# Performance work log

Measured on AMD Instinct MI355X. Metric: run time of the kernel, lower is better.

Reference implementation:

```python
import jax, jax.numpy as jnp
import numpy as np
import math

CHUNK = 32
NS_STEPS = 5
MAX_GNORM = 10.0


def _normalize(x, eps=1e-12):
    n = jnp.linalg.norm(x, axis=-1, keepdims=True)
    return x / jnp.maximum(n, eps)


def _poly(x):  # poly_degree = 2: [x, x^2] / sqrt(2)
    return jnp.concatenate([x, x * x], axis=-1) / math.sqrt(2.0)


def _ns5(G):
    # Muon-style Newton-Schulz orthogonalization (quintic, 5 steps)
    a, b, c = 3.4445, -4.7750, 2.0315
    t = G.shape[0] > G.shape[1]
    X = G.T if t else G
    X = X / (jnp.linalg.norm(X) + 1e-7)
    for _ in range(NS_STEPS):
        A = X @ X.T
        B = b * A + c * (A @ A)
        X = a * X + B @ X
    return X.T if t else X


def _clip_mean(g):
    # per-sample grad-norm clipping to MAX_GNORM, then mean over samples
    n = g.shape[0]
    norms = jnp.maximum(jnp.linalg.norm(g.reshape(n, -1), axis=1), 1e-8)
    scale = jnp.maximum(norms / MAX_GNORM, 1.0)
    return jnp.mean(g / scale.reshape((n,) + (1,) * (g.ndim - 1)), axis=0)


def _mem_fwd(W0, W1, z):  # MemoryMLP depth=2, gelu (exact) between layers
    return jax.nn.gelu(z @ W0, approximate=False) @ W1


def setup_inputs() -> dict:
    key = jax.random.key(0)
    ks = jax.random.split(key, 16)
    B, S, D, M, P, H = 2, 1024, 2048, 512, 1024, 2048
    w = lambda k, shape, fan_in: jax.random.normal(k, shape, jnp.float32) / np.float32(np.sqrt(fan_in))
    return {
        "x": jax.random.normal(ks[0], (B, S, D), jnp.float32),
        "Wk": w(ks[1], (M, D), D),
        "Wv": w(ks[2], (M, D), D),
        "Wq": w(ks[3], (M, D), D),
        "Wout": w(ks[4], (D, M), M),
        "w_lr": w(ks[5], (1, D), D), "b_lr": jnp.full((1,), -4.0, jnp.float32),
        "w_mom": w(ks[6], (1, D), D), "b_mom": jnp.full((1,), 1.0, jnp.float32),
        "w_dec": w(ks[7], (1, D), D), "b_dec": jnp.full((1,), -3.0, jnp.float32),
        "w_gate": w(ks[8], (1, D), D), "b_gate": jnp.full((1,), -1.0, jnp.float32),
        "Wmem0": w(ks[9], (P, H), P),
        "Wmem1": w(ks[10], (H, P), H),
        "Wmemout": w(ks[11], (P, M), P),
        "Wvexp": w(ks[12], (M, P), M),
    }


def reference(x, Wk, Wv, Wq, Wout, w_lr, b_lr, w_mom, b_mom, w_dec, b_dec,
              w_gate, b_gate, Wmem0, Wmem1, Wmemout, Wvexp):
    # Inference path (torch.is_grad_enabled() == False): chunked ATLAS update.
    B, S, D = x.shape
    NC = S // CHUNK

    k = _normalize(x @ Wk.T)          # (B,S,M)
    v = x @ Wv.T                       # (B,S,M)
    q = _normalize(x @ Wq.T)          # (B,S,M)
    kp = _poly(k)                      # (B,S,P)
    qp = _poly(q)                      # (B,S,P)
    vexp = v @ Wvexp                   # v_expand: (B,S,P)

    gate = lambda w, b: jax.nn.sigmoid(jnp.einsum('bsd,od->bso', x, w) + b)
    lr, mom, dec, og = gate(w_lr, b_lr), gate(w_mom, b_mom), gate(w_dec, b_dec), gate(w_gate, b_gate)

    cmean = lambda t: t[..., 0].reshape(B, NC, CHUNK).mean(axis=(0, 2))  # per-chunk scalar
    lr_c, mom_c, dec_c = cmean(lr), cmean(mom), cmean(dec)

    chunks = lambda t: t.reshape(B, NC, CHUNK, t.shape[-1]).transpose(1, 0, 2, 3)  # (NC,B,C,F)
    qc, kc, vc = chunks(qp), chunks(kp), chunks(vexp)

    def loss_fn(params, kk, vv):  # ||M(k) - v||^2 per sample
        W0_, W1_ = params
        pred = jax.nn.gelu(kk @ W0_, approximate=False) @ W1_
        return jnp.sum((pred - vv) ** 2)

    grad_fn = jax.vmap(jax.grad(loss_fn), in_axes=((None, None), 0, 0))

    def step(carry, xs):
        W0, W1, S0, S1 = carry
        qch, kch, vch, lrc, momc, decc = xs
        retr = _mem_fwd(W0, W1, qch) @ Wmemout  # retrieve with pre-update params: (B,C,M)
        kf = kch.reshape(-1, kch.shape[-1])
        vf = vch.reshape(-1, vch.shape[-1])
        g0, g1 = grad_fn((W0, W1), kf, vf)      # per-sample grads
        g0, g1 = _clip_mean(g0), _clip_mean(g1)
        s0 = momc * S0 - lrc * g0                # surprise momentum
        s1 = momc * S1 - lrc * g1
        W0n = (1.0 - decc) * W0 + _ns5(s0) * lrc # forget gate + orthogonalized step
        W1n = (1.0 - decc) * W1 + _ns5(s1) * lrc
        return (W0n, W1n, s0, s1), retr

    init = (Wmem0, Wmem1, jnp.zeros_like(Wmem0), jnp.zeros_like(Wmem1))
    _, retrs = jax.lax.scan(step, init, (qc, kc, vc, lr_c, mom_c, dec_c))
    retrieved = retrs.transpose(1, 0, 2, 3).reshape(B, S, -1)  # (B,S,M)
    delta = retrieved @ Wout.T
    return x + delta * og
```

## Files before the change

### kernel.cpp

```cpp
#include <hip/hip_runtime.h>


typedef unsigned short us;
typedef __attribute__((ext_vector_type(8))) short s16x8;
typedef __attribute__((ext_vector_type(8))) unsigned short u16x8;
typedef __attribute__((ext_vector_type(4))) float f32x4;

#define MKP 72

__device__ __forceinline__ float gelu_f(float x) {
  return 0.5f * x * (1.0f + erff(x * 0.70710678118654752f));
}
__device__ __forceinline__ float gelu_grad_f(float x) {
  float cdf = 0.5f * (1.0f + erff(x * 0.70710678118654752f));
  float pdf = 0.3989422804014327f * expf(-0.5f * x * x);
  return cdf + x * pdf;
}
__device__ __forceinline__ float sigmoid_f(float x) { return 1.0f / (1.0f + expf(-x)); }

__device__ __forceinline__ us f2bf(float f) {
  union { float f; unsigned u; } v; v.f = f;
  unsigned r = (v.u + 0x7FFFu + ((v.u >> 16) & 1u)) >> 16;
  return (us)r;
}
__device__ __forceinline__ float bf2f(us h) {
  union { unsigned u; float f; } v; v.u = ((unsigned)h) << 16;
  return v.f;
}
__device__ __forceinline__ int cm_map(int n) {
  return ((n & 1023) >> 5) * 64 + (n >> 10) * 32 + (n & 31);
}
__device__ __forceinline__ size_t pf_off(int r, int k, int KB) {
  return ((size_t)(r >> 4) * KB + (k >> 5)) * 512 + ((k >> 3) & 3) * 128 + (r & 15) * 8 + (k & 7);
}

__device__ __forceinline__ float block_reduce_sum(float v, float* red) {
  int t = threadIdx.x;
  red[t] = v; __syncthreads();
  for (int s = blockDim.x >> 1; s > 0; s >>= 1) {
    if (t < s) red[t] += red[t + s];
    __syncthreads();
  }
  float r = red[0];
  __syncthreads();
  return r;
}

__device__ __forceinline__ void gemm_pk(const us* __restrict__ A,
                                        const us* __restrict__ B, int KB,
                                        int lane, int m0, int n0,
                                        f32x4 (&acc)[4][4]) {
  const us* am[4];
  const us* bm[4];
#pragma unroll
  for (int q = 0; q < 4; ++q) {
    am[q] = A + (size_t)((m0 >> 4) + q) * KB * 512 + lane * 8;
    bm[q] = B + (size_t)((n0 >> 4) + q) * KB * 512 + lane * 8;
  }
#pragma unroll
  for (int i = 0; i < 4; ++i)
#pragma unroll
    for (int j = 0; j < 4; ++j) acc[i][j] = (f32x4){0.f, 0.f, 0.f, 0.f};
  u16x8 a0[4], b0[4], a1[4], b1[4];
#pragma unroll
  for (int q = 0; q < 4; ++q) {
    a0[q] = *(const u16x8*)(am[q]);
    b0[q] = *(const u16x8*)(bm[q]);
    a1[q] = *(const u16x8*)(am[q] + 512);
    b1[q] = *(const u16x8*)(bm[q] + 512);
  }
  for (int kb = 0; kb < KB; kb += 2) {
#pragma unroll
    for (int mi = 0; mi < 4; ++mi)
#pragma unroll
      for (int ni = 0; ni < 4; ++ni)
        acc[mi][ni] = __builtin_amdgcn_mfma_f32_16x16x32_bf16(
            (s16x8)a0[mi], (s16x8)b0[ni], acc[mi][ni], 0, 0, 0);
    if (kb + 2 < KB) {
#pragma unroll
      for (int q = 0; q < 4; ++q) {
        a0[q] = *(const u16x8*)(am[q] + (size_t)(kb + 2) * 512);
        b0[q] = *(const u16x8*)(bm[q] + (size_t)(kb + 2) * 512);
      }
    }
#pragma unroll
    for (int mi = 0; mi < 4; ++mi)
#pragma unroll
      for (int ni = 0; ni < 4; ++ni)
        acc[mi][ni] = __builtin_amdgcn_mfma_f32_16x16x32_bf16(
            (s16x8)a1[mi], (s16x8)b1[ni], acc[mi][ni], 0, 0, 0);
    if (kb + 3 < KB) {
#pragma unroll
      for (int q = 0; q < 4; ++q) {
        a1[q] = *(const u16x8*)(am[q] + (size_t)(kb + 3) * 512);
        b1[q] = *(const u16x8*)(bm[q] + (size_t)(kb + 3) * 512);
      }
    }
  }
}

template<int EPI, int TM, int TN>
__global__ __launch_bounds__(256)
void mgp_k(const us* __restrict__ Aq, const us* __restrict__ Bq,
           us* __restrict__ Cq, us* __restrict__ C2q, const us* __restrict__ Eq,
           int K, int N, float c1, float c2,
           long sA, long sB, long sC, long sE) {
  __shared__ __align__(16) us ct[4 * 64 * 72];
  const int tid = threadIdx.x;
  const int wave = tid >> 6, lane = tid & 63;
  const int l15 = lane & 15, l4 = lane >> 4;
  const int wm = (wave >> 1) * 64, wn = (wave & 1) * 64;
  const int TPB = TM * TN;
  const int t = blockIdx.x;
  const int bz = t / TPB;
  const int ti = t - bz * TPB;
  const int m0 = (ti / TN) * 128 + wm;
  const int n0 = (ti % TN) * 128 + wn;

  const us* A = Aq + (size_t)bz * sA;
  const us* B = Bq + (size_t)bz * sB;
  us* C = Cq + (size_t)bz * sC;
  us* C2 = C2q + (size_t)bz * sC;
  const us* E = Eq + (size_t)bz * sE;
  const int KB = K >> 5;

  f32x4 acc[4][4];
  gemm_pk(A, B, KB, lane, m0, n0, acc);

  us* cw = ct + wave * 64 * 72;
#pragma unroll
  for (int mi = 0; mi < 4; ++mi)
#pragma unroll
    for (int i = 0; i < 4; ++i)
#pragma unroll
      for (int ni = 0; ni < 4; ++ni)
        cw[(mi * 16 + l4 * 4 + i) * 72 + ni * 16 + l15] = f2bf(acc[mi][ni][i]);

  if constexpr (EPI == 20 || EPI == 21) {
    const int KC = N >> 5;
#pragma unroll
    for (int q = 0; q < 8; ++q) {
      u16x8 v = *(const u16x8*)&cw[lane * 72 + q * 8];
      size_t off = pf_off(m0 + lane, n0 + q * 8, KC);
      if constexpr (EPI == 21) {
        u16x8 e = *(const u16x8*)(E + off);
        u16x8 o;
#pragma unroll
        for (int w = 0; w < 8; ++w) o[w] = f2bf(c1 * bf2f(v[w]) + c2 * bf2f(e[w]));
        *(u16x8*)(C + off) = o;
      } else {
        *(u16x8*)(C + off) = v;
      }
    }
  } else if constexpr (EPI == 23) {
#pragma unroll
    for (int q = 0; q < 8; ++q) {
      size_t off = pf_off(m0 + lane, n0 + q * 8, 64);
      u16x8 v = *(const u16x8*)&cw[lane * 72 + q * 8];
      u16x8 e = *(const u16x8*)(E + off);
      u16x8 o;
#pragma unroll
      for (int w = 0; w < 8; ++w) o[w] = f2bf(bf2f(v[w]) + c1 * bf2f(e[w]));
      *(u16x8*)&cw[lane * 72 + q * 8] = o;
      *(u16x8*)(C + off) = o;
    }
#pragma unroll
    for (int q = 0; q < 8; ++q) {
      u16x8 o;
#pragma unroll
      for (int w = 0; w < 8; ++w) o[w] = cw[(q * 8 + w) * 72 + lane];
      size_t offT = pf_off(n0 + lane, m0 + q * 8, 32);
      *(u16x8*)(C2 + offT) = o;
    }
  } else {
#pragma unroll
    for (int q = 0; q < 8; ++q) {
      size_t off = pf_off(m0 + lane, n0 + q * 8, 64);
      u16x8 v = *(const u16x8*)&cw[lane * 72 + q * 8];
      u16x8 e = *(const u16x8*)(E + off);
      u16x8 o;
#pragma unroll
      for (int w = 0; w < 8; ++w) o[w] = f2bf(bf2f(v[w]) + c1 * bf2f(e[w]));
      *(u16x8*)(C + (size_t)(m0 + lane) * 2048 + n0 + q * 8) = o;
    }
  }
}

template<int EPI, int TM, int TN>
static void mgp(hipStream_t st, const us* A, const us* B, us* C, us* C2,
                const us* E, int K, int N, float c1, float c2,
                long sA, long sB, long sC, long sE) {
  dim3 g(TM * TN * 2), b(256);
  hipLaunchKernelGGL((mgp_k<EPI, TM, TN>), g, b, 0, st, A, B, C, C2, E,
                     K, N, c1, c2, sA, sB, sC, sE);
}

template<int EPI>
__device__ __forceinline__ void epilogue(f32x4 (&acc)[4][4], int m0, int n0,
    int l15, int l4, void* Cq, void* C2, const void* Eq,
    const float* FX, const float* OG, const float* cp, int cidx,
    int ldc, int lde, float c1, float c2) {
#pragma unroll
  for (int mi = 0; mi < 4; ++mi) {
#pragma unroll
    for (int i = 0; i < 4; ++i) {
      int grow = m0 + mi * 16 + l4 * 4 + i;
#pragma unroll
      for (int ni = 0; ni < 4; ++ni) {
        int col = n0 + ni * 16 + l15;
        float v = acc[mi][ni][i];
        if constexpr (EPI == 5) {
          ((us*)Cq)[(size_t)grow * ldc + col] = f2bf(v);
        } else if constexpr (EPI == 7) {
          ((float*)Cq)[(size_t)grow * ldc + col] = v;
        } else if constexpr (EPI == 8) {
          ((us*)Cq)[(size_t)grow * ldc + col] = f2bf(gelu_f(v));
          if (m0 >= 64)
            ((float*)C2)[(size_t)(grow - 64) * ldc + col] = gelu_grad_f(v);
        } else if constexpr (EPI == 9) {
          if (m0 < 64)
            ((us*)Cq)[(size_t)grow * ldc + col] = f2bf(v);
          else
            ((us*)Cq)[(size_t)grow * ldc + col] =
                f2bf(2.0f * (v - ((const float*)Eq)[(size_t)(grow - 64) * lde + col]));
        } else if constexpr (EPI == 13) {
          ((float*)Cq)[(size_t)grow * ldc + col] =
              v * ((const float*)Eq)[(size_t)grow * lde + col];
        } else if constexpr (EPI == 14) {
          float* C = (float*)Cq;
          float old = C[(size_t)grow * ldc + col];
          C[(size_t)grow * ldc + col] = cp[cidx * 3 + 1] * old - cp[cidx * 3 + 0] * v;
        } else if constexpr (EPI == 15) {
          ((float*)Cq)[(size_t)grow * ldc + col] =
              FX[(size_t)grow * ldc + col] + v * OG[grow];
        } else if constexpr (EPI == 17) {
          int crow = cm_map(grow);
          ((float*)Cq)[(size_t)crow * ldc + col] = v;
        }
      }
    }
  }
}

template<int EPI, int TA, int DUAL, int AG>
__global__ __launch_bounds__(64)
void mg_k(const us* __restrict__ Aq, const us* __restrict__ A2,
          const us* __restrict__ Bq, void* __restrict__ Cq,
          void* __restrict__ C2, const void* __restrict__ Eq,
          const float* __restrict__ FX, const float* __restrict__ OG,
          const float* __restrict__ cp, int cidx,
          int M, int N, int K, int lda, int ldb, int ldc, int lde,
          float c1, float c2) {
  __shared__ __align__(16) us As[64 * MKP];
  __shared__ __align__(16) us Bs[64 * MKP];
  const us* A = Aq;
  const us* B = Bq;
  const int t = threadIdx.x;
  const int m0 = blockIdx.y * 64, n0 = blockIdx.x * 64;
  if constexpr (DUAL) { if (m0 >= 64) A = A2; }
  const int mA0 = DUAL ? (m0 & 63) : m0;
  const int l15 = t & 15, l4 = t >> 4;

  f32x4 acc[4][4];
#pragma unroll
  for (int i = 0; i < 4; ++i)
#pragma unroll
    for (int j = 0; j < 4; ++j) acc[i][j] = (f32x4){0.f, 0.f, 0.f, 0.f};

  const int srw = t >> 3;
  const int sck = (t & 7) * 8;

  u16x8 ra[8], rb[8];
  auto LDA = [&](int k0) {
#pragma unroll
    for (int p = 0; p < 8; ++p) {
      if constexpr (TA == 0) {
        int row = srw + p * 8;
        int srow;
        if constexpr (AG) srow = cm_map(m0 + row); else srow = mA0 + row;
        ra[p] = *(const u16x8*)(A + (size_t)srow * lda + k0 + sck);
      } else {
        ra[p] = *(const u16x8*)(A + (size_t)(k0 + srw + p * 8) * lda + mA0 + sck);
      }
    }
  };
  auto LDB = [&](int k0) {
#pragma unroll
    for (int p = 0; p < 8; ++p)
      rb[p] = *(const u16x8*)(B + (size_t)(n0 + srw + p * 8) * ldb + k0 + sck);
  };

  LDA(0); LDB(0);
  for (int k0 = 0; k0 < K; k0 += 64) {
    if constexpr (TA == 0) {
#pragma unroll
      for (int p = 0; p < 8; ++p)
        *(u16x8*)&As[(srw + p * 8) * MKP + sck] = ra[p];
    } else {
#pragma unroll
      for (int p = 0; p < 8; ++p) {
        int kk = srw + p * 8;
#pragma unroll
        for (int j = 0; j < 8; ++j) As[(sck + j) * MKP + kk] = ra[p][j];
      }
    }
#pragma unroll
    for (int p = 0; p < 8; ++p)
      *(u16x8*)&Bs[(srw + p * 8) * MKP + sck] = rb[p];
    if (k0 + 64 < K) { LDA(k0 + 64); LDB(k0 + 64); }
#pragma unroll
    for (int ks = 0; ks < 2; ++ks) {
      s16x8 af[4], bf[4];
#pragma unroll
      for (int mi = 0; mi < 4; ++mi)
        af[mi] = *(const s16x8*)&As[(mi * 16 + l15) * MKP + ks * 32 + l4 * 8];
#pragma unroll
      for (int ni = 0; ni < 4; ++ni)
        bf[ni] = *(const s16x8*)&Bs[(ni * 16 + l15) * MKP + ks * 32 + l4 * 8];
#pragma unroll
      for (int mi = 0; mi < 4; ++mi)
#pragma unroll
        for (int ni = 0; ni < 4; ++ni)
          acc[mi][ni] = __builtin_amdgcn_mfma_f32_16x16x32_bf16(af[mi], bf[ni], acc[mi][ni], 0, 0, 0);
    }
  }

  epilogue<EPI>(acc, m0, n0, l15, l4, Cq, C2, Eq, FX, OG, cp, cidx,
                ldc, lde, c1, c2);
}

template<int EPI, int TA = 0, int DUAL = 0, int AG = 0>
static void mg(hipStream_t st, const us* A, const us* A2, const us* B,
               void* C, void* C2, const void* E,
               const float* FX, const float* OG, const float* cp, int cidx,
               int M, int N, int K, int lda, int ldb, int ldc, int lde,
               float c1 = 0.f, float c2 = 0.f) {
  dim3 g(N / 64, M / 64, 1), b(64);
  hipLaunchKernelGGL((mg_k<EPI, TA, DUAL, AG>), g, b, 0, st, A, A2, B, C, C2, E,
                     FX, OG, cp, cidx, M, N, K, lda, ldb, ldc, lde, c1, c2);
}

__global__ void scalepk2_k(const float* __restrict__ S0, const float* __restrict__ S1,
                           const float* __restrict__ inv01,
                           us* __restrict__ XP, us* __restrict__ XTP) {
  __shared__ float tile[32][33];
  const long SB2c = 2097152;
  int z = blockIdx.z;
  float s = inv01[z];
  int tx = threadIdx.x, ty = threadIdx.y;
  int r0, c0;
  const float* S;
  if (z == 0) { S = S0; c0 = blockIdx.x * 32; r0 = blockIdx.y * 32; }
  else        { S = S1; r0 = blockIdx.x * 32; c0 = blockIdx.y * 32; }
  int C = (z == 0) ? 2048 : 1024;
#pragma unroll
  for (int j = 0; j < 4; ++j)
    tile[ty + 8 * j][tx] = S[(size_t)(r0 + ty + 8 * j) * C + c0 + tx] * s;
  __syncthreads();
  us* xp = XP + (size_t)z * SB2c;
  us* xt = XTP + (size_t)z * SB2c;
  int t = ty * 32 + tx;
  if (t < 128) {
    int rh = t >> 2, cc = t & 3;
    u16x8 v;
#pragma unroll
    for (int e = 0; e < 8; ++e) v[e] = f2bf(tile[rh][cc * 8 + e]);
    if (z == 0) {
      *(u16x8*)(xp + pf_off(r0 + rh, c0 + cc * 8, 64)) = v;
    } else {
      *(u16x8*)(xt + pf_off(r0 + rh, c0 + cc * 8, 32)) = v;
    }
  } else {
    int ch = (t - 128) >> 2, rc = (t - 128) & 3;
    u16x8 v;
#pragma unroll
    for (int e = 0; e < 8; ++e) v[e] = f2bf(tile[rc * 8 + e][ch]);
    if (z == 0) {
      *(u16x8*)(xt + pf_off(c0 + ch, r0 + rc * 8, 32)) = v;
    } else {
      *(u16x8*)(xp + pf_off(c0 + ch, r0 + rc * 8, 64)) = v;
    }
  }
}


__global__ __launch_bounds__(256) void conv_k(const float* __restrict__ in,
                                              us* __restrict__ out, int n) {
  for (int i = blockIdx.x * 256 + threadIdx.x; i < n; i += gridDim.x * 256)
    out[i] = f2bf(in[i]);
}

__global__ void tconv_k(const float* __restrict__ in, us* __restrict__ out, int R, int C) {
  __shared__ float tile[32][33];
  int c0 = blockIdx.x * 32, r0 = blockIdx.y * 32;
  int tx = threadIdx.x, ty = threadIdx.y;
#pragma unroll
  for (int j = 0; j < 4; ++j)
    tile[ty + 8 * j][tx] = in[(size_t)(r0 + ty + 8 * j) * C + c0 + tx];
  __syncthreads();
#pragma unroll
  for (int j = 0; j < 4; ++j)
    out[(size_t)(c0 + ty + 8 * j) * R + r0 + tx] = f2bf(tile[tx][ty + 8 * j]);
}


__global__ __launch_bounds__(256) void polynorm2_k(const float* __restrict__ lin,
                                                   us* __restrict__ outp) {
  __shared__ float red[256];
  int n = blockIdx.x, t = threadIdx.x;
  int rowp = cm_map(n);
  float s = 0.f;
  for (int f = t; f < 512; f += 256) { float v = lin[(size_t)n * 512 + f]; s += v * v; }
  float tot = block_reduce_sum(s, red);
  float sc = 1.0f / fmaxf(sqrtf(tot), 1e-12f);
  const float is2 = 0.70710678118654752f;
  for (int f = t; f < 512; f += 256) {
    float v = lin[(size_t)n * 512 + f] * sc;
    outp[(size_t)rowp * 1024 + f] = f2bf(v * is2);
    outp[(size_t)rowp * 1024 + 512 + f] = f2bf(v * v * is2);
  }
}

__global__ __launch_bounds__(256) void gates_k(const float* __restrict__ x,
    const float* __restrict__ wlr, const float* __restrict__ blr,
    const float* __restrict__ wmom, const float* __restrict__ bmom,
    const float* __restrict__ wdec, const float* __restrict__ bdec,
    const float* __restrict__ wgate, const float* __restrict__ bgate,
    float* __restrict__ lrv, float* __restrict__ momv,
    float* __restrict__ decv, float* __restrict__ og) {
  __shared__ float red[256];
  int n = blockIdx.x, t = threadIdx.x;
  float s0 = 0.f, s1 = 0.f, s2 = 0.f, s3 = 0.f;
  for (int d = t; d < 2048; d += 256) {
    float xv = x[(size_t)n * 2048 + d];
    s0 += xv * wlr[d]; s1 += xv * wmom[d]; s2 += xv * wdec[d]; s3 += xv * wgate[d];
  }
  float r0 = block_reduce_sum(s0, red);
  float r1 = block_reduce_sum(s1, red);
  float r2 = block_reduce_sum(s2, red);
  float r3 = block_reduce_sum(s3, red);
  if (t == 0) {
    lrv[n] = sigmoid_f(r0 + blr[0]);
    momv[n] = sigmoid_f(r1 + bmom[0]);
    decv[n] = sigmoid_f(r2 + bdec[0]);
    og[n] = sigmoid_f(r3 + bgate[0]);
  }
}

__global__ void chunk_means_k(const float* __restrict__ lrv, const float* __restrict__ momv,
                              const float* __restrict__ decv, float* __restrict__ cp) {
  int c = blockIdx.x, t = threadIdx.x;
  int n = ((t >> 5) << 10) + c * 32 + (t & 31);
  float a = lrv[n], b = momv[n], d = decv[n];
  for (int off = 32; off > 0; off >>= 1) {
    a += __shfl_down(a, off);
    b += __shfl_down(b, off);
    d += __shfl_down(d, off);
  }
  if (t == 0) {
    cp[c * 3 + 0] = a * (1.f / 64.f);
    cp[c * 3 + 1] = b * (1.f / 64.f);
    cp[c * 3 + 2] = d * (1.f / 64.f);
  }
}

__global__ __launch_bounds__(256) void sampnorm2_k(const us* __restrict__ kp_b,
                                                   const float* __restrict__ dh,
                                                   const us* __restrict__ hab,
                                                   const us* __restrict__ pr,
                                                   float* __restrict__ w0inv,
                                                   float* __restrict__ w1inv, int c) {
  __shared__ float red[256];
  int i = blockIdx.x, t = threadIdx.x;
  int row = c * 64 + i;
  float sk = 0.f, sr = 0.f, sdh = 0.f, sa = 0.f;
  for (int p = t; p < 1024; p += 256) {
    float v = bf2f(kp_b[(size_t)row * 1024 + p]); sk += v * v;
    v = bf2f(pr[(size_t)(64 + i) * 1024 + p]); sr += v * v;
  }
  for (int h = t; h < 2048; h += 256) {
    float v = dh[(size_t)i * 2048 + h]; sdh += v * v;
    v = bf2f(hab[(size_t)(64 + i) * 2048 + h]); sa += v * v;
  }
  float tk = block_reduce_sum(sk, red);
  float tdh = block_reduce_sum(sdh, red);
  float ta = block_reduce_sum(sa, red);
  float tr = block_reduce_sum(sr, red);
  if (t == 0) {
    float n0 = fmaxf(sqrtf(tk) * sqrtf(tdh), 1e-8f);
    w0inv[i] = 1.0f / (64.0f * fmaxf(n0 * 0.1f, 1.0f));
    float n1 = fmaxf(sqrtf(ta) * sqrtf(tr), 1e-8f);
    w1inv[i] = 1.0f / (64.0f * fmaxf(n1 * 0.1f, 1.0f));
  }
}

template<int INF32>
__global__ void wtrans_k(const void* __restrict__ in, const float* __restrict__ w,
                         us* __restrict__ out, int C, int ldin) {
  __shared__ float tile[32][33];
  int c0 = blockIdx.x * 32, r0 = blockIdx.y * 32;
  int tx = threadIdx.x, ty = threadIdx.y;
#pragma unroll
  for (int j = 0; j < 4; ++j) {
    int r = r0 + ty + 8 * j, cc = c0 + tx;
    float v;
    if constexpr (INF32) v = ((const float*)in)[(size_t)r * ldin + cc];
    else v = bf2f(((const us*)in)[(size_t)r * ldin + cc]);
    tile[ty + 8 * j][tx] = v * w[r];
  }
  __syncthreads();
#pragma unroll
  for (int j = 0; j < 4; ++j)
    out[(size_t)(c0 + ty + 8 * j) * 64 + r0 + tx] = f2bf(tile[tx][ty + 8 * j]);
}

__global__ __launch_bounds__(256) void frob2_k(const float* __restrict__ s0,
                                               const float* __restrict__ s1, int n,
                                               float* __restrict__ parts) {
  __shared__ float red[256];
  const float* s = blockIdx.z ? s1 : s0;
  float acc = 0.f;
  for (int i = blockIdx.x * 256 + threadIdx.x; i < n; i += gridDim.x * 256) {
    float v = s[i]; acc += v * v;
  }
  float r = block_reduce_sum(acc, red);
  if (threadIdx.x == 0) parts[blockIdx.z * 256 + blockIdx.x] = r;
}

__global__ __launch_bounds__(256) void frob_fin2_k(const float* __restrict__ parts,
                                                   float* __restrict__ inv) {
  __shared__ float red[256];
  float r = block_reduce_sum(parts[blockIdx.x * 256 + threadIdx.x], red);
  if (threadIdx.x == 0) inv[blockIdx.x] = 1.0f / (sqrtf(r) + 1e-7f);
}

__global__ void wupd0_k(float* __restrict__ W0, const us* __restrict__ X,
                        us* __restrict__ W0bT, const float* __restrict__ cp, int c) {
  __shared__ float tl[32][33];
  float lr = cp[c * 3 + 0], om = 1.0f - cp[c * 3 + 2];
  int c0 = blockIdx.x * 32, r0 = blockIdx.y * 32;
  int tx = threadIdx.x, ty = threadIdx.y;
#pragma unroll
  for (int j = 0; j < 4; ++j) {
    int r = r0 + ty + 8 * j, h = c0 + tx;
    size_t idx = (size_t)r * 2048 + h;
    float v = om * W0[idx] + lr * bf2f(X[idx]);
    W0[idx] = v;
    tl[ty + 8 * j][tx] = v;
  }
  __syncthreads();
#pragma unroll
  for (int j = 0; j < 4; ++j)
    W0bT[(size_t)(c0 + ty + 8 * j) * 1024 + r0 + tx] = f2bf(tl[tx][ty + 8 * j]);
}

__global__ void wupd1_k(float* __restrict__ W1, const us* __restrict__ X2,
                        us* __restrict__ W1b, us* __restrict__ W1bT,
                        const float* __restrict__ cp, int c) {
  __shared__ float tX[32][33];
  __shared__ float t2[32][33];
  float lr = cp[c * 3 + 0], om = 1.0f - cp[c * 3 + 2];
  int h0 = blockIdx.x * 32, p0 = blockIdx.y * 32;
  int tx = threadIdx.x, ty = threadIdx.y;
#pragma unroll
  for (int j = 0; j < 4; ++j)
    tX[ty + 8 * j][tx] = bf2f(X2[(size_t)(p0 + ty + 8 * j) * 2048 + h0 + tx]);
  __syncthreads();
#pragma unroll
  for (int j = 0; j < 4; ++j) {
    int h = h0 + ty + 8 * j, p = p0 + tx;
    size_t idx = (size_t)h * 1024 + p;
    float v = om * W1[idx] + lr * tX[tx][ty + 8 * j];
    W1[idx] = v;
    W1b[idx] = f2bf(v);
    t2[tx][ty + 8 * j] = v;
  }
  __syncthreads();
#pragma unroll
  for (int j = 0; j < 4; ++j)
    W1bT[(size_t)(p0 + ty + 8 * j) * 2048 + h0 + tx] = f2bf(t2[ty + 8 * j][tx]);
}


extern "C" void kernel_launch(void* const* d_in, const int* in_sizes, int n_in,
                              void* d_out, int out_size, void* d_ws, size_t ws_size,
                              hipStream_t stream) {
  const float* x = (const float*)d_in[0];
  const float* Wk = (const float*)d_in[1];
  const float* Wv = (const float*)d_in[2];
  const float* Wq = (const float*)d_in[3];
  const float* Wout = (const float*)d_in[4];
  const float* w_lr = (const float*)d_in[5];
  const float* b_lr = (const float*)d_in[6];
  const float* w_mom = (const float*)d_in[7];
  const float* b_mom = (const float*)d_in[8];
  const float* w_dec = (const float*)d_in[9];
  const float* b_dec = (const float*)d_in[10];
  const float* w_gate = (const float*)d_in[11];
  const float* b_gate = (const float*)d_in[12];
  const float* Wmem0 = (const float*)d_in[13];
  const float* Wmem1 = (const float*)d_in[14];
  const float* Wmemout = (const float*)d_in[15];
  const float* Wvexp = (const float*)d_in[16];
  float* out = (float*)d_out;
  (void)n_in; (void)in_sizes; (void)out_size;

  const long F = 1048576;
  const long BIG = 2097152;
  const long SB2 = 2097152, SB1 = 1048576;
  float* ws = (float*)d_ws;
  if (ws_size < (size_t)25043464 * sizeof(float)) return;

  us* kp_b   = (us*)ws;
  us* qp_b   = (us*)(ws + F);
  float* vexp = ws + 2 * F;
  float* W0  = ws + 4 * F;
  float* W1  = ws + 6 * F;
  float* S0  = ws + 8 * F;
  float* S1  = ws + 10 * F;
  us* XPong  = (us*)(ws + 12 * F);
  us* XTPong = (us*)(ws + 14 * F);
  us* XPing  = (us*)(ws + 16 * F);
  us* AP     = (us*)(ws + 18 * F);
  float* SCR = ws + 19 * F;
  us* XTPing = (us*)(ws + 20 * F);
  us* BP     = (us*)(ws + 22 * F);
  us* W0bT   = (us*)(ws + 20 * F);
  us* W1bT   = (us*)(ws + 21 * F);
  us* W1b    = (us*)(ws + 22 * F);
  us* WmoT   = (us*)(ws + 23 * F);
  us* retrv  = (us*)(ws + 23 * F + 262144);
  float* smal = ws + 23 * F + 262144 + 524288;
  float* og   = smal;
  float* lrv  = og + 2048;
  float* momv = lrv + 2048;
  float* decv = momv + 2048;
  float* cpb  = decv + 2048;
  float* w0inv = cpb + 128;
  float* w1inv = w0inv + 64;
  float* parts = w1inv + 64;
  float* inv01 = parts + 512;

  us* xb   = XPong;
  us* Wkb  = XTPong;
  us* Wqb  = XTPong + 1048576;
  us* Wvb  = XTPong + 2097152;
  us* vlin = XPing;
  us* WvexpT = XPing + 1048576;
  us* Woutb = AP;
  float* lin = SCR;
  us* hab   = (us*)SCR;
  float* gp = SCR + 131072;
  us* pr    = (us*)(SCR + 262144);
  float* dh = SCR + 327680;
  us* dhT   = (us*)(SCR + 458752);
  us* rbwT  = (us*)(SCR + 524288);
  us* Xfin  = XPong;

  const float NSa = 3.4445f, NSb = -4.7750f, NSc = 2.0315f;

  hipMemcpyAsync(W0, Wmem0, (size_t)BIG * 4, hipMemcpyDeviceToDevice, stream);
  hipMemcpyAsync(W1, Wmem1, (size_t)BIG * 4, hipMemcpyDeviceToDevice, stream);
  hipMemsetAsync(S0, 0, (size_t)BIG * 4, stream);
  hipMemsetAsync(S1, 0, (size_t)BIG * 4, stream);
  hipLaunchKernelGGL(tconv_k, dim3(64, 32), dim3(32, 8), 0, stream, Wmem0, W0bT, 1024, 2048);
  hipLaunchKernelGGL(conv_k, dim3(1024), dim3(256), 0, stream, Wmem1, W1b, (int)BIG);
  hipLaunchKernelGGL(tconv_k, dim3(32, 64), dim3(32, 8), 0, stream, Wmem1, W1bT, 2048, 1024);
  hipLaunchKernelGGL(tconv_k, dim3(16, 32), dim3(32, 8), 0, stream, Wmemout, WmoT, 1024, 512);
  hipLaunchKernelGGL(tconv_k, dim3(32, 16), dim3(32, 8), 0, stream, Wvexp, WvexpT, 512, 1024);
  hipLaunchKernelGGL(conv_k, dim3(2048), dim3(256), 0, stream, x, xb, 2048 * 2048);
  hipLaunchKernelGGL(conv_k, dim3(512), dim3(256), 0, stream, Wk, Wkb, 512 * 2048);
  hipLaunchKernelGGL(conv_k, dim3(512), dim3(256), 0, stream, Wq, Wqb, 512 * 2048);
  hipLaunchKernelGGL(conv_k, dim3(512), dim3(256), 0, stream, Wv, Wvb, 512 * 2048);

  mg<7>(stream, xb, nullptr, Wkb, lin, nullptr, nullptr, nullptr, nullptr, nullptr, 0,
        2048, 512, 2048, 2048, 2048, 512, 0);
  hipLaunchKernelGGL(polynorm2_k, dim3(2048), dim3(256), 0, stream, lin, kp_b);
  mg<7>(stream, xb, nullptr, Wqb, lin, nullptr, nullptr, nullptr, nullptr, nullptr, 0,
        2048, 512, 2048, 2048, 2048, 512, 0);
  hipLaunchKernelGGL(polynorm2_k, dim3(2048), dim3(256), 0, stream, lin, qp_b);
  mg<5>(stream, xb, nullptr, Wvb, vlin, nullptr, nullptr, nullptr, nullptr, nullptr, 0,
        2048, 512, 2048, 2048, 2048, 512, 0);
  mg<17>(stream, vlin, nullptr, WvexpT, vexp, nullptr, nullptr, nullptr, nullptr, nullptr, 0,
         2048, 1024, 512, 512, 512, 1024, 0);

  hipLaunchKernelGGL(gates_k, dim3(2048), dim3(256), 0, stream, x,
                     w_lr, b_lr, w_mom, b_mom, w_dec, b_dec, w_gate, b_gate,
                     lrv, momv, decv, og);
  hipLaunchKernelGGL(chunk_means_k, dim3(32), dim3(64), 0, stream, lrv, momv, decv, cpb);

  for (int c = 0; c < 32; ++c) {
    const us* kp_c = kp_b + (size_t)c * 64 * 1024;
    const us* qp_c = qp_b + (size_t)c * 64 * 1024;
    const float* vexp_c = vexp + (size_t)c * 64 * 1024;
    mg<8, 0, 1>(stream, qp_c, kp_c, W0bT, hab, gp, nullptr, nullptr, nullptr, nullptr, 0,
                128, 2048, 1024, 1024, 1024, 2048, 0);
    mg<9>(stream, hab, nullptr, W1bT, pr, nullptr, vexp_c, nullptr, nullptr, nullptr, 0,
          128, 1024, 2048, 2048, 2048, 1024, 1024);
    mg<5>(stream, pr, nullptr, WmoT, retrv + (size_t)c * 64 * 512, nullptr, nullptr,
          nullptr, nullptr, nullptr, 0, 64, 512, 1024, 1024, 1024, 512, 0);
    mg<13>(stream, pr + 64 * 1024, nullptr, W1b, dh, nullptr, gp, nullptr, nullptr, nullptr, 0,
           64, 2048, 1024, 1024, 1024, 2048, 2048);
    hipLaunchKernelGGL(sampnorm2_k, dim3(64), dim3(256), 0, stream,
                       kp_b, dh, hab, pr, w0inv, w1inv, c);
    hipLaunchKernelGGL((wtrans_k<1>), dim3(64, 2), dim3(32, 8), 0, stream, dh, w0inv, dhT, 2048, 2048);
    hipLaunchKernelGGL((wtrans_k<0>), dim3(32, 2), dim3(32, 8), 0, stream, pr + 64 * 1024, w1inv,
                       rbwT, 1024, 1024);
    mg<14, 1>(stream, kp_c, nullptr, dhT, S0, nullptr, nullptr, nullptr, nullptr, cpb, c,
              1024, 2048, 64, 1024, 64, 2048, 0);
    mg<14, 1>(stream, hab + 64 * 2048, nullptr, rbwT, S1, nullptr, nullptr, nullptr, nullptr, cpb, c,
              2048, 1024, 64, 2048, 64, 1024, 0);

    hipLaunchKernelGGL(frob2_k, dim3(256, 1, 2), dim3(256), 0, stream, S0, S1, (int)BIG, parts);
    hipLaunchKernelGGL(frob_fin2_k, dim3(2), dim3(256), 0, stream, parts, inv01);
    hipLaunchKernelGGL(scalepk2_k, dim3(64, 32, 2), dim3(32, 8), 0, stream,
                       S0, S1, inv01, XPing, XTPing);

    us* xpA[2] = {XPing, XPong};
    us* xtA[2] = {XTPing, XTPong};
    int cur = 0;
    for (int it = 0; it < 5; ++it) {
      const us* XPc = xpA[cur];
      const us* XTPc = xtA[cur];
      int nxt = cur ^ 1;
      mgp<20, 8, 8>(stream, XPc, XPc, AP, nullptr, nullptr, 2048, 1024,
                    0.f, 0.f, SB2, SB2, SB1, 0);
      mgp<21, 8, 8>(stream, AP, AP, BP, nullptr, AP, 1024, 1024,
                    NSc, NSb, SB1, SB1, SB1, SB1);
      if (it < 4) {
        mgp<23, 8, 16>(stream, BP, XTPc, xpA[nxt], xtA[nxt], XPc, 1024, 2048,
                       NSa, 0.f, SB1, SB2, SB2, SB2);
        cur = nxt;
      } else {
        mgp<24, 8, 16>(stream, BP, XTPc, Xfin, nullptr, XPc, 1024, 2048,
                       NSa, 0.f, SB1, SB2, SB2, SB2);
      }
    }
    hipLaunchKernelGGL(wupd0_k, dim3(64, 32), dim3(32, 8), 0, stream, W0, Xfin, W0bT, cpb, c);
    hipLaunchKernelGGL(wupd1_k, dim3(64, 32), dim3(32, 8), 0, stream, W1, Xfin + SB2, W1b, W1bT, cpb, c);
  }

  hipLaunchKernelGGL(conv_k, dim3(1024), dim3(256), 0, stream, Wout, Woutb, 2048 * 512);
  mg<15, 0, 0, 1>(stream, retrv, nullptr, Woutb, out, nullptr, nullptr, x, og, nullptr, 0,
                  2048, 2048, 512, 512, 512, 2048, 0);
}
```

Before: 15.80 ms.

## Exploit symmetry in Newton-Schulz Gram products and merge per-chunk kernel launches

The X·Xᵀ and A·A products in the Newton-Schulz loop are symmetric, so only upper-triangular 128x128 tiles are computed and off-diagonal tiles are mirrored into the transposed position. This roughly halves the MFMA work for two of the three GEMMs per iteration. The two transpose kernels and the two momentum-update GEMMs are each merged into a single launch to cut launch overhead. The triangular tile index is decoded with a small loop per block, and mirrored writes add some uncoalesced-style transposed stores.

```diff
diff --git a/kernel.cpp b/kernel.cpp
--- a/kernel.cpp
+++ b/kernel.cpp
@@ -99,7 +99,7 @@
   }
 }
 
-template<int EPI, int TM, int TN>
+template<int EPI, int TRI, int TM, int TN>
 __global__ __launch_bounds__(256)
 void mgp_k(const us* __restrict__ Aq, const us* __restrict__ Bq,
            us* __restrict__ Cq, us* __restrict__ C2q, const us* __restrict__ Eq,
@@ -110,12 +110,29 @@
   const int wave = tid >> 6, lane = tid & 63;
   const int l15 = lane & 15, l4 = lane >> 4;
   const int wm = (wave >> 1) * 64, wn = (wave & 1) * 64;
-  const int TPB = TM * TN;
-  const int t = blockIdx.x;
-  const int bz = t / TPB;
-  const int ti = t - bz * TPB;
-  const int m0 = (ti / TN) * 128 + wm;
-  const int n0 = (ti % TN) * 128 + wn;
+  int bz, m0, n0;
+  bool mir = false;
+  if constexpr (TRI) {
+    const int per = TM * (TM + 1) / 2;
+    int t = blockIdx.x;
+    bz = t / per;
+    int ti = t - bz * per;
+    int m0t, n0t;
+    if (ti < TM) { m0t = n0t = ti * 128; }
+    else {
+      int p = ti - TM, i = 0;
+      while (p >= TM - 1 - i) { p -= TM - 1 - i; ++i; }
+      m0t = i * 128; n0t = (i + 1 + p) * 128; mir = true;
+    }
+    m0 = m0t + wm; n0 = n0t + wn;
+  } else {
+    const int TPB = TM * TN;
+    int t = blockIdx.x;
+    bz = t / TPB;
+    int ti = t - bz * TPB;
+    m0 = (ti / TN) * 128 + wm;
+    n0 = (ti % TN) * 128 + wn;
+  }
 
   const us* A = Aq + (size_t)bz * sA;
   const us* B = Bq + (size_t)bz * sB;
@@ -152,6 +169,24 @@
         *(u16x8*)(C + off) = v;
       }
     }
+    if (TRI && mir) {
+#pragma unroll
+      for (int q = 0; q < 8; ++q) {
+        u16x8 vT;
+#pragma unroll
+        for (int w = 0; w < 8; ++w) vT[w] = cw[(q * 8 + w) * 72 + lane];
+        size_t offM = pf_off(n0 + lane, m0 + q * 8, KC);
+        if constexpr (EPI == 21) {
+          u16x8 e = *(const u16x8*)(E + offM);
+          u16x8 o;
+#pragma unroll
+          for (int w = 0; w < 8; ++w) o[w] = f2bf(c1 * bf2f(vT[w]) + c2 * bf2f(e[w]));
+          *(u16x8*)(C + offM) = o;
+        } else {
+          *(u16x8*)(C + offM) = vT;
+        }
+      }
+    }
   } else if constexpr (EPI == 23) {
 #pragma unroll
     for (int q = 0; q < 8; ++q) {
@@ -186,12 +221,12 @@
   }
 }
 
-template<int EPI, int TM, int TN>
+template<int EPI, int TRI, int TM, int TN>
 static void mgp(hipStream_t st, const us* A, const us* B, us* C, us* C2,
                 const us* E, int K, int N, float c1, float c2,
                 long sA, long sB, long sC, long sE) {
-  dim3 g(TM * TN * 2), b(256);
-  hipLaunchKernelGGL((mgp_k<EPI, TM, TN>), g, b, 0, st, A, B, C, C2, E,
+  dim3 g(TRI ? TM * (TM + 1) : TM * TN * 2), b(256);
+  hipLaunchKernelGGL((mgp_k<EPI, TRI, TM, TN>), g, b, 0, st, A, B, C, C2, E,
                      K, N, c1, c2, sA, sB, sC, sE);
 }
 
@@ -243,6 +278,87 @@
 }
 
 template<int EPI, int TA, int DUAL, int AG>
+__device__ __forceinline__ void mg_body(const us* __restrict__ A0,
+    const us* __restrict__ A2, const us* __restrict__ B,
+    void* __restrict__ Cq, void* __restrict__ C2, const void* __restrict__ Eq,
+    const float* __restrict__ FX, const float* __restrict__ OG,
+    const float* __restrict__ cp, int cidx, int m0, int n0,
+    int K, int lda, int ldb, int ldc, int lde, float c1, float c2,
+    us* As, us* Bs, int t) {
+  const us* A = A0;
+  if constexpr (DUAL) { if (m0 >= 64) A = A2; }
+  const int mA0 = DUAL ? (m0 & 63) : m0;
+  const int l15 = t & 15, l4 = t >> 4;
+
+  f32x4 acc[4][4];
+#pragma unroll
+  for (int i = 0; i < 4; ++i)
+#pragma unroll
+    for (int j = 0; j < 4; ++j) acc[i][j] = (f32x4){0.f, 0.f, 0.f, 0.f};
+
+  const int srw = t >> 3;
+  const int sck = (t & 7) * 8;
+
+  u16x8 ra[8], rb[8];
+  auto LDA = [&](int k0) {
+#pragma unroll
+    for (int p = 0; p < 8; ++p) {
+      if constexpr (TA == 0) {
+        int row = srw + p * 8;
+        int srow;
+        if constexpr (AG) srow = cm_map(m0 + row); else srow = mA0 + row;
+        ra[p] = *(const u16x8*)(A + (size_t)srow * lda + k0 + sck);
+      } else {
+        ra[p] = *(const u16x8*)(A + (size_t)(k0 + srw + p * 8) * lda + mA0 + sck);
+      }
+    }
+  };
+  auto LDB = [&](int k0) {
+#pragma unroll
+    for (int p = 0; p < 8; ++p)
+      rb[p] = *(const u16x8*)(B + (size_t)(n0 + srw + p * 8) * ldb + k0 + sck);
+  };
+
+  LDA(0); LDB(0);
+  for (int k0 = 0; k0 < K; k0 += 64) {
+    if constexpr (TA == 0) {
+#pragma unroll
+      for (int p = 0; p < 8; ++p)
+        *(u16x8*)&As[(srw + p * 8) * MKP + sck] = ra[p];
+    } else {
+#pragma unroll
+      for (int p = 0; p < 8; ++p) {
+        int kk = srw + p * 8;
+#pragma unroll
+        for (int j = 0; j < 8; ++j) As[(sck + j) * MKP + kk] = ra[p][j];
+      }
+    }
+#pragma unroll
+    for (int p = 0; p < 8; ++p)
+      *(u16x8*)&Bs[(srw + p * 8) * MKP + sck] = rb[p];
+    if (k0 + 64 < K) { LDA(k0 + 64); LDB(k0 + 64); }
+#pragma unroll
+    for (int ks = 0; ks < 2; ++ks) {
+      s16x8 af[4], bf[4];
+#pragma unroll
+      for (int mi = 0; mi < 4; ++mi)
+        af[mi] = *(const s16x8*)&As[(mi * 16 + l15) * MKP + ks * 32 + l4 * 8];
+#pragma unroll
+      for (int ni = 0; ni < 4; ++ni)
+        bf[ni] = *(const s16x8*)&Bs[(ni * 16 + l15) * MKP + ks * 32 + l4 * 8];
+#pragma unroll
+      for (int mi = 0; mi < 4; ++mi)
+#pragma unroll
+        for (int ni = 0; ni < 4; ++ni)
+          acc[mi][ni] = __builtin_amdgcn_mfma_f32_16x16x32_bf16(af[mi], bf[ni], acc[mi][ni], 0, 0, 0);
+    }
+  }
+
+  epilogue<EPI>(acc, m0, n0, l15, l4, Cq, C2, Eq, FX, OG, cp, cidx,
+                ldc, lde, c1, c2);
+}
+
+template<int EPI, int TA, int DUAL, int AG>
 __global__ __launch_bounds__(64)
 void mg_k(const us* __restrict__ Aq, const us* __restrict__ A2,
           const us* __restrict__ Bq, void* __restrict__ Cq,
@@ -253,80 +369,9 @@
           float c1, float c2) {
   __shared__ __align__(16) us As[64 * MKP];
   __shared__ __align__(16) us Bs[64 * MKP];
-  const us* A = Aq;
-  const us* B = Bq;
-  const int t = threadIdx.x;
-  const int m0 = blockIdx.y * 64, n0 = blockIdx.x * 64;
-  if constexpr (DUAL) { if (m0 >= 64) A = A2; }
-  const int mA0 = DUAL ? (m0 & 63) : m0;
-  const int l15 = t & 15, l4 = t >> 4;
-
-  f32x4 acc[4][4];
-#pragma unroll
-  for (int i = 0; i < 4; ++i)
-#pragma unroll
-    for (int j = 0; j < 4; ++j) acc[i][j] = (f32x4){0.f, 0.f, 0.f, 0.f};
-
-  const int srw = t >> 3;
-  const int sck = (t & 7) * 8;
-
-  u16x8 ra[8], rb[8];
-  auto LDA = [&](int k0) {
-#pragma unroll
-    for (int p = 0; p < 8; ++p) {
-      if constexpr (TA == 0) {
-        int row = srw + p * 8;
-        int srow;
-        if constexpr (AG) srow = cm_map(m0 + row); else srow = mA0 + row;
-        ra[p] = *(const u16x8*)(A + (size_t)srow * lda + k0 + sck);
-      } else {
-        ra[p] = *(const u16x8*)(A + (size_t)(k0 + srw + p * 8) * lda + mA0 + sck);
-      }
-    }
-  };
-  auto LDB = [&](int k0) {
-#pragma unroll
-    for (int p = 0; p < 8; ++p)
-      rb[p] = *(const u16x8*)(B + (size_t)(n0 + srw + p * 8) * ldb + k0 + sck);
-  };
-
-  LDA(0); LDB(0);
-  for (int k0 = 0; k0 < K; k0 += 64) {
-    if constexpr (TA == 0) {
-#pragma unroll
-      for (int p = 0; p < 8; ++p)
-        *(u16x8*)&As[(srw + p * 8) * MKP + sck] = ra[p];
-    } else {
-#pragma unroll
-      for (int p = 0; p < 8; ++p) {
-        int kk = srw + p * 8;
-#pragma unroll
-        for (int j = 0; j < 8; ++j) As[(sck + j) * MKP + kk] = ra[p][j];
-      }
-    }
-#pragma unroll
-    for (int p = 0; p < 8; ++p)
-      *(u16x8*)&Bs[(srw + p * 8) * MKP + sck] = rb[p];
-    if (k0 + 64 < K) { LDA(k0 + 64); LDB(k0 + 64); }
-#pragma unroll
-    for (int ks = 0; ks < 2; ++ks) {
-      s16x8 af[4], bf[4];
-#pragma unroll
-      for (int mi = 0; mi < 4; ++mi)
-        af[mi] = *(const s16x8*)&As[(mi * 16 + l15) * MKP + ks * 32 + l4 * 8];
-#pragma unroll
-      for (int ni = 0; ni < 4; ++ni)
-        bf[ni] = *(const s16x8*)&Bs[(ni * 16 + l15) * MKP + ks * 32 + l4 * 8];
-#pragma unroll
-      for (int mi = 0; mi < 4; ++mi)
-#pragma unroll
-        for (int ni = 0; ni < 4; ++ni)
-          acc[mi][ni] = __builtin_amdgcn_mfma_f32_16x16x32_bf16(af[mi], bf[ni], acc[mi][ni], 0, 0, 0);
-    }
-  }
-
-  epilogue<EPI>(acc, m0, n0, l15, l4, Cq, C2, Eq, FX, OG, cp, cidx,
-                ldc, lde, c1, c2);
+  mg_body<EPI, TA, DUAL, AG>(Aq, A2, Bq, Cq, C2, Eq, FX, OG, cp, cidx,
+                             blockIdx.y * 64, blockIdx.x * 64, K, lda, ldb,
+                             ldc, lde, c1, c2, As, Bs, threadIdx.x);
 }
 
 template<int EPI, int TA = 0, int DUAL = 0, int AG = 0>
@@ -338,6 +383,60 @@
   dim3 g(N / 64, M / 64, 1), b(64);
   hipLaunchKernelGGL((mg_k<EPI, TA, DUAL, AG>), g, b, 0, st, A, A2, B, C, C2, E,
                      FX, OG, cp, cidx, M, N, K, lda, ldb, ldc, lde, c1, c2);
+}
+
+__global__ __launch_bounds__(64)
+void mg2_k(const us* __restrict__ kp_c, const us* __restrict__ dhT,
+           float* __restrict__ S0, const us* __restrict__ habk,
+           const us* __restrict__ rbwT, float* __restrict__ S1,
+           const float* __restrict__ cp, int c) {
+  __shared__ __align__(16) us As[64 * MKP];
+  __shared__ __align__(16) us Bs[64 * MKP];
+  int bid = blockIdx.x;
+  if (bid < 512) {
+    int m0 = (bid >> 5) * 64, n0 = (bid & 31) * 64;
+    mg_body<14, 1, 0, 0>(kp_c, nullptr, dhT, S0, nullptr, nullptr,
+                         nullptr, nullptr, cp, c, m0, n0,
+                         64, 1024, 64, 2048, 0, 0.f, 0.f, As, Bs, threadIdx.x);
+  } else {
+    int b2 = bid - 512;
+    int m0 = (b2 >> 4) * 64, n0 = (b2 & 15) * 64;
+    mg_body<14, 1, 0, 0>(habk, nullptr, rbwT, S1, nullptr, nullptr,
+                         nullptr, nullptr, cp, c, m0, n0,
+                         64, 2048, 64, 1024, 0, 0.f, 0.f, As, Bs, threadIdx.x);
+  }
+}
+
+__global__ void wt2_k(const float* __restrict__ dh, const float* __restrict__ w0inv,
+                      us* __restrict__ dhT, const us* __restrict__ prg,
+                      const float* __restrict__ w1inv, us* __restrict__ rbwT) {
+  __shared__ float tile[32][33];
+  int bid = blockIdx.x;
+  int tx = threadIdx.x, ty = threadIdx.y;
+  int c0, r0, ldin;
+  const float* wv;
+  us* outp;
+  bool f32in;
+  const void* in;
+  if (bid < 128) {
+    in = dh; wv = w0inv; outp = dhT; ldin = 2048; f32in = true;
+    c0 = (bid & 63) * 32; r0 = (bid >> 6) * 32;
+  } else {
+    int b2 = bid - 128;
+    in = prg; wv = w1inv; outp = rbwT; ldin = 1024; f32in = false;
+    c0 = (b2 & 31) * 32; r0 = (b2 >> 5) * 32;
+  }
+#pragma unroll
+  for (int j = 0; j < 4; ++j) {
+    int r = r0 + ty + 8 * j, cc = c0 + tx;
+    float v = f32in ? ((const float*)in)[(size_t)r * ldin + cc]
+                    : bf2f(((const us*)in)[(size_t)r * ldin + cc]);
+    tile[ty + 8 * j][tx] = v * wv[r];
+  }
+  __syncthreads();
+#pragma unroll
+  for (int j = 0; j < 4; ++j)
+    outp[(size_t)(c0 + ty + 8 * j) * 64 + r0 + tx] = f2bf(tile[tx][ty + 8 * j]);
 }
 
 __global__ void scalepk2_k(const float* __restrict__ S0, const float* __restrict__ S1,
@@ -492,26 +591,6 @@
     float n1 = fmaxf(sqrtf(ta) * sqrtf(tr), 1e-8f);
     w1inv[i] = 1.0f / (64.0f * fmaxf(n1 * 0.1f, 1.0f));
   }
-}
-
-template<int INF32>
-__global__ void wtrans_k(const void* __restrict__ in, const float* __restrict__ w,
-                         us* __restrict__ out, int C, int ldin) {
-  __shared__ float tile[32][33];
-  int c0 = blockIdx.x * 32, r0 = blockIdx.y * 32;
-  int tx = threadIdx.x, ty = threadIdx.y;
-#pragma unroll
-  for (int j = 0; j < 4; ++j) {
-    int r = r0 + ty + 8 * j, cc = c0 + tx;
-    float v;
-    if constexpr (INF32) v = ((const float*)in)[(size_t)r * ldin + cc];
-    else v = bf2f(((const us*)in)[(size_t)r * ldin + cc]);
-    tile[ty + 8 * j][tx] = v * w[r];
-  }
-  __syncthreads();
-#pragma unroll
-  for (int j = 0; j < 4; ++j)
-    out[(size_t)(c0 + ty + 8 * j) * 64 + r0 + tx] = f2bf(tile[tx][ty + 8 * j]);
 }
 
 __global__ __launch_bounds__(256) void frob2_k(const float* __restrict__ s0,
@@ -703,13 +782,10 @@
            64, 2048, 1024, 1024, 1024, 2048, 2048);
     hipLaunchKernelGGL(sampnorm2_k, dim3(64), dim3(256), 0, stream,
                        kp_b, dh, hab, pr, w0inv, w1inv, c);
-    hipLaunchKernelGGL((wtrans_k<1>), dim3(64, 2), dim3(32, 8), 0, stream, dh, w0inv, dhT, 2048, 2048);
-    hipLaunchKernelGGL((wtrans_k<0>), dim3(32, 2), dim3(32, 8), 0, stream, pr + 64 * 1024, w1inv,
-                       rbwT, 1024, 1024);
-    mg<14, 1>(stream, kp_c, nullptr, dhT, S0, nullptr, nullptr, nullptr, nullptr, cpb, c,
-              1024, 2048, 64, 1024, 64, 2048, 0);
-    mg<14, 1>(stream, hab + 64 * 2048, nullptr, rbwT, S1, nullptr, nullptr, nullptr, nullptr, cpb, c,
-              2048, 1024, 64, 2048, 64, 1024, 0);
+    hipLaunchKernelGGL(wt2_k, dim3(192), dim3(32, 8), 0, stream,
+                       dh, w0inv, dhT, pr + 64 * 1024, w1inv, rbwT);
+    hipLaunchKernelGGL(mg2_k, dim3(1024), dim3(64), 0, stream,
+                       kp_c, dhT, S0, hab + 64 * 2048, rbwT, S1, cpb, c);
 
     hipLaunchKernelGGL(frob2_k, dim3(256, 1, 2), dim3(256), 0, stream, S0, S1, (int)BIG, parts);
     hipLaunchKernelGGL(frob_fin2_k, dim3(2), dim3(256), 0, stream, parts, inv01);
@@ -723,17 +799,17 @@
       const us* XPc = xpA[cur];
       const us* XTPc = xtA[cur];
       int nxt = cur ^ 1;
-      mgp<20, 8, 8>(stream, XPc, XPc, AP, nullptr, nullptr, 2048, 1024,
-                    0.f, 0.f, SB2, SB2, SB1, 0);
-      mgp<21, 8, 8>(stream, AP, AP, BP, nullptr, AP, 1024, 1024,
-                    NSc, NSb, SB1, SB1, SB1, SB1);
+      mgp<20, 1, 8, 8>(stream, XPc, XPc, AP, nullptr, nullptr, 2048, 1024,
+                       0.f, 0.f, SB2, SB2, SB1, 0);
+      mgp<21, 1, 8, 8>(stream, AP, AP, BP, nullptr, AP, 1024, 1024,
+                       NSc, NSb, SB1, SB1, SB1, SB1);
       if (it < 4) {
-        mgp<23, 8, 16>(stream, BP, XTPc, xpA[nxt], xtA[nxt], XPc, 1024, 2048,
-                       NSa, 0.f, SB1, SB2, SB2, SB2);
+        mgp<23, 0, 8, 16>(stream, BP, XTPc, xpA[nxt], xtA[nxt], XPc, 1024, 2048,
+                          NSa, 0.f, SB1, SB2, SB2, SB2);
         cur = nxt;
       } else {
-        mgp<24, 8, 16>(stream, BP, XTPc, Xfin, nullptr, XPc, 1024, 2048,
-                       NSa, 0.f, SB1, SB2, SB2, SB2);
+        mgp<24, 0, 8, 16>(stream, BP, XTPc, Xfin, nullptr, XPc, 1024, 2048,
+                          NSa, 0.f, SB1, SB2, SB2, SB2);
       }
     }
     hipLaunchKernelGGL(wupd0_k, dim3(64, 32), dim3(32, 8), 0, stream, W0, Xfin, W0bT, cpb, c);
```

Result: slower. 17.03 ms (+7.8%).
